# Kernel optimization log

Measured on AMD Instinct MI355X. Metric: run time of the kernel, lower is better.

The kernel has to match this reference:

```python
import jax, jax.numpy as jnp
import numpy as np

EPS = 1e-05


def setup_inputs() -> dict:
    key = jax.random.key(0)
    k1, k2, k3 = jax.random.split(key, 3)
    B, S, D = 8, 4096, 1024  # batch, row(seq_len), col(d_model)
    x = jax.random.normal(k1, (B, S, D), dtype=jnp.float32)
    alpha = jnp.ones((D,), dtype=jnp.float32)
    beta = jnp.zeros((D,), dtype=jnp.float32)
    return {"x": x, "alpha": alpha, "beta": beta}


def reference(x, alpha, beta):
    # Faithful translation of LayerNorm_v2.forward, including its quirks:
    #  - statistics computed ONLY from batch element 0 (loop over x_t[0])
    #  - nonstandard running-mean recurrence: mean = (mean + data) / i
    #  - var accumulates (data - mean_i)^2 against the *updated* running mean
    #  - Bessel-style divide by (col - 1)
    # x: [B, S, D]; stats are per-row (per S), computed by streaming over D.
    B, S, D = x.shape
    data = x[0].T  # [D, S] -> loop iterates over the D (col) dimension

    def step(carry, d):
        mean, var, i = carry
        mean = (mean + d) / i          # quirky running mean
        var = var + jnp.square(d - mean)
        return (mean, var, i + 1.0), None

    init = (jnp.zeros((S,), x.dtype), jnp.zeros((S,), x.dtype),
            jnp.asarray(1.0, x.dtype))
    (mean, var, _), _ = jax.lax.scan(step, init, data)
    var = var / (D - 1)
    mean = mean[:, None]  # [S, 1]
    var = var[:, None]    # [S, 1]
    # broadcast stats from batch 0 across the whole batch, per-feature affine
    return alpha * (x - mean) / jnp.sqrt(var + EPS) + beta
```

## Files before the change

kernel.cpp:

```cpp
#include <hip/hip_runtime.h>
#include <math.h>

#define BB 8
#define SS 4096
#define DD 1024
#define EPSF 1e-5f

typedef float f32x4 __attribute__((ext_vector_type(4)));

__device__ __forceinline__ f32x4 shfl4(const f32x4 v, int lane) {
    f32x4 r;
    r.x = __shfl(v.x, lane, 64);
    r.y = __shfl(v.y, lane, 64);
    r.z = __shfl(v.z, lane, 64);
    r.w = __shfl(v.w, lane, 64);
    return r;
}
__device__ __forceinline__ f32x4 shfl4_up1(const f32x4 v) {
    f32x4 r;
    r.x = __shfl_up(v.x, 1, 64);
    r.y = __shfl_up(v.y, 1, 64);
    r.z = __shfl_up(v.z, 1, 64);
    r.w = __shfl_up(v.w, 1, 64);
    return r;
}

__global__ __launch_bounds__(256) void fused_ln_kernel(
    const float* __restrict__ x,
    const float* __restrict__ alpha,
    const float* __restrict__ beta,
    float* __restrict__ out)
{
    const int L   = threadIdx.x & 63;
    const int wv  = threadIdx.x >> 6;
    const int row = (blockIdx.x << 2) | wv;
    const size_t row4   = (size_t)row * (DD / 4);
    const size_t batch4 = (size_t)SS * (DD / 4);

    const f32x4* __restrict__ xp = reinterpret_cast<const f32x4*>(x);
    f32x4*       __restrict__ op = reinterpret_cast<f32x4*>(out);

    f32x4 v[4];
#pragma unroll
    for (int c = 0; c < 4; ++c)
        v[c] = xp[row4 + L + 64 * c];

    size_t cb = batch4 + row4;
    f32x4 cur[4];
#pragma unroll
    for (int c = 0; c < 4; ++c)
        cur[c] = xp[cb + L + 64 * c];

    const f32x4* __restrict__ a4 = reinterpret_cast<const f32x4*>(alpha);
    const f32x4* __restrict__ b4 = reinterpret_cast<const f32x4*>(beta);
    f32x4 av[4], bv[4];
#pragma unroll
    for (int c = 0; c < 4; ++c) { av[c] = a4[L + 64 * c]; bv[c] = b4[L + 64 * c]; }

    float var    = 0.0f;
    float m_last = 0.0f;
#pragma unroll
    for (int c = 0; c < 4; ++c) {
        const f32x4 up1 = shfl4_up1(v[c]);
        const float u2z = __shfl_up(v[c].z, 2, 64);
        const float u2w = __shfl_up(v[c].w, 2, 64);
        f32x4 wrap1 = {0.f, 0.f, 0.f, 0.f};
        float wz = 0.f, ww = 0.f;
        if (c > 0) {
            wrap1 = shfl4(v[c - 1], 63);
            wz = __shfl(v[c - 1].z, 62, 64);
            ww = __shfl(v[c - 1].w, 62, 64);
        }

        const float jf = (float)(256 * c + 4 * L);
        float m;
        if (c == 0 && L == 0) {
            m = 0.0f;
        } else if (c == 0 && L == 1) {
            m = up1.w * 0.25f + up1.z * (1.0f / 12.0f)
              + (up1.y + up1.x) * (1.0f / 24.0f);
        } else {
            const f32x4 w25 = (L == 0) ? wrap1 : up1;
            float w0, w1;
            if (L >= 2)      { w0 = u2z;     w1 = u2w;     }
            else if (L == 1) { w0 = wrap1.z; w1 = wrap1.w; }
            else             { w0 = wz;      w1 = ww;      }
            float acc = w0;
            acc = fmaf(acc, __builtin_amdgcn_rcpf(jf - 5.0f), w1);
            acc = fmaf(acc, __builtin_amdgcn_rcpf(jf - 4.0f), w25.x);
            acc = fmaf(acc, __builtin_amdgcn_rcpf(jf - 3.0f), w25.y);
            acc = fmaf(acc, __builtin_amdgcn_rcpf(jf - 2.0f), w25.z);
            acc = fmaf(acc, __builtin_amdgcn_rcpf(jf - 1.0f), w25.w);
            m = acc * __builtin_amdgcn_rcpf(jf);
        }

        const float dd[4] = { v[c].x, v[c].y, v[c].z, v[c].w };
#pragma unroll
        for (int t = 0; t < 4; ++t) {
            m = (m + dd[t]) * __builtin_amdgcn_rcpf(jf + (float)(t + 1));
            const float df = dd[t] - m;
            var = fmaf(df, df, var);
        }
        m_last = m;
    }

#pragma unroll
    for (int off = 32; off >= 1; off >>= 1) var += __shfl_xor(var, off, 64);
    const float mf = __shfl(m_last, 63, 64);
    const float r  = rsqrtf(var * (1.0f / 1023.0f) + EPSF);

    f32x4 sc[4], bs[4];
#pragma unroll
    for (int c = 0; c < 4; ++c) {
        sc[c].x = av[c].x * r;  sc[c].y = av[c].y * r;
        sc[c].z = av[c].z * r;  sc[c].w = av[c].w * r;
        bs[c].x = fmaf(-mf, sc[c].x, bv[c].x);
        bs[c].y = fmaf(-mf, sc[c].y, bv[c].y);
        bs[c].z = fmaf(-mf, sc[c].z, bv[c].z);
        bs[c].w = fmaf(-mf, sc[c].w, bv[c].w);
    }

#pragma unroll
    for (int c = 0; c < 4; ++c) {
        f32x4 o;
        o.x = fmaf(v[c].x, sc[c].x, bs[c].x);
        o.y = fmaf(v[c].y, sc[c].y, bs[c].y);
        o.z = fmaf(v[c].z, sc[c].z, bs[c].z);
        o.w = fmaf(v[c].w, sc[c].w, bs[c].w);
        __builtin_nontemporal_store(o, op + row4 + L + 64 * c);
    }

#pragma unroll
    for (int b = 1; b <= 6; ++b) {
        f32x4 nxt[4];
#pragma unroll
        for (int c = 0; c < 4; ++c)
            nxt[c] = xp[cb + batch4 + L + 64 * c];
#pragma unroll
        for (int c = 0; c < 4; ++c) {
            f32x4 o;
            o.x = fmaf(cur[c].x, sc[c].x, bs[c].x);
            o.y = fmaf(cur[c].y, sc[c].y, bs[c].y);
            o.z = fmaf(cur[c].z, sc[c].z, bs[c].z);
            o.w = fmaf(cur[c].w, sc[c].w, bs[c].w);
            __builtin_nontemporal_store(o, op + cb + L + 64 * c);
        }
#pragma unroll
        for (int c = 0; c < 4; ++c) cur[c] = nxt[c];
        cb += batch4;
    }
#pragma unroll
    for (int c = 0; c < 4; ++c) {
        f32x4 o;
        o.x = fmaf(cur[c].x, sc[c].x, bs[c].x);
        o.y = fmaf(cur[c].y, sc[c].y, bs[c].y);
        o.z = fmaf(cur[c].z, sc[c].z, bs[c].z);
        o.w = fmaf(cur[c].w, sc[c].w, bs[c].w);
        __builtin_nontemporal_store(o, op + cb + L + 64 * c);
    }
}

extern "C" void kernel_launch(void* const* d_in, const int* in_sizes, int n_in,
                              void* d_out, int out_size, void* d_ws, size_t ws_size,
                              hipStream_t stream) {
    (void)in_sizes; (void)n_in; (void)out_size; (void)d_ws; (void)ws_size;
    const float* x     = (const float*)d_in[0];
    const float* alpha = (const float*)d_in[1];
    const float* beta  = (const float*)d_in[2];
    float* out = (float*)d_out;

    hipLaunchKernelGGL(fused_ln_kernel, dim3(SS / 4), dim3(256), 0, stream,
                       x, alpha, beta, out);
}
```

Baseline: 237.1 us.

## Split each row's batch broadcast across two waves and raise occupancy

Each row is now handled by two wavefronts instead of one. Both waves redundantly compute the batch-0 statistics, then one writes batches 0-3 and the other batches 4-7, doubling the grid. It also drops the software prefetch of the next batch, loads alpha/beta after the reduction, uses nontemporal loads, and sets launch_bounds min blocks to 8 to raise occupancy. The cost is doubled batch-0 reads and statistics compute, traded for more parallelism and memory-level concurrency.

```diff
diff --git a/kernel.cpp b/kernel.cpp
--- a/kernel.cpp
+++ b/kernel.cpp
@@ -25,15 +25,16 @@
     return r;
 }
 
-__global__ __launch_bounds__(256) void fused_ln_kernel(
+__global__ __launch_bounds__(256, 8) void fused_ln_kernel(
     const float* __restrict__ x,
     const float* __restrict__ alpha,
     const float* __restrict__ beta,
     float* __restrict__ out)
 {
-    const int L   = threadIdx.x & 63;
-    const int wv  = threadIdx.x >> 6;
-    const int row = (blockIdx.x << 2) | wv;
+    const int L    = threadIdx.x & 63;
+    const int wv   = threadIdx.x >> 6;
+    const int half = wv & 1;
+    const int row  = (blockIdx.x << 1) | (wv >> 1);
     const size_t row4   = (size_t)row * (DD / 4);
     const size_t batch4 = (size_t)SS * (DD / 4);
 
@@ -43,19 +44,7 @@
     f32x4 v[4];
 #pragma unroll
     for (int c = 0; c < 4; ++c)
-        v[c] = xp[row4 + L + 64 * c];
-
-    size_t cb = batch4 + row4;
-    f32x4 cur[4];
-#pragma unroll
-    for (int c = 0; c < 4; ++c)
-        cur[c] = xp[cb + L + 64 * c];
-
-    const f32x4* __restrict__ a4 = reinterpret_cast<const f32x4*>(alpha);
-    const f32x4* __restrict__ b4 = reinterpret_cast<const f32x4*>(beta);
-    f32x4 av[4], bv[4];
-#pragma unroll
-    for (int c = 0; c < 4; ++c) { av[c] = a4[L + 64 * c]; bv[c] = b4[L + 64 * c]; }
+        v[c] = __builtin_nontemporal_load(xp + row4 + L + 64 * c);
 
     float var    = 0.0f;
     float m_last = 0.0f;
@@ -109,54 +98,66 @@
     const float mf = __shfl(m_last, 63, 64);
     const float r  = rsqrtf(var * (1.0f / 1023.0f) + EPSF);
 
+    const f32x4* __restrict__ a4 = reinterpret_cast<const f32x4*>(alpha);
+    const f32x4* __restrict__ b4 = reinterpret_cast<const f32x4*>(beta);
     f32x4 sc[4], bs[4];
 #pragma unroll
     for (int c = 0; c < 4; ++c) {
-        sc[c].x = av[c].x * r;  sc[c].y = av[c].y * r;
-        sc[c].z = av[c].z * r;  sc[c].w = av[c].w * r;
-        bs[c].x = fmaf(-mf, sc[c].x, bv[c].x);
-        bs[c].y = fmaf(-mf, sc[c].y, bv[c].y);
-        bs[c].z = fmaf(-mf, sc[c].z, bv[c].z);
-        bs[c].w = fmaf(-mf, sc[c].w, bv[c].w);
+        const f32x4 av = a4[L + 64 * c];
+        const f32x4 bv = b4[L + 64 * c];
+        sc[c].x = av.x * r;  sc[c].y = av.y * r;
+        sc[c].z = av.z * r;  sc[c].w = av.w * r;
+        bs[c].x = fmaf(-mf, sc[c].x, bv.x);
+        bs[c].y = fmaf(-mf, sc[c].y, bv.y);
+        bs[c].z = fmaf(-mf, sc[c].z, bv.z);
+        bs[c].w = fmaf(-mf, sc[c].w, bv.w);
     }
 
-#pragma unroll
-    for (int c = 0; c < 4; ++c) {
-        f32x4 o;
-        o.x = fmaf(v[c].x, sc[c].x, bs[c].x);
-        o.y = fmaf(v[c].y, sc[c].y, bs[c].y);
-        o.z = fmaf(v[c].z, sc[c].z, bs[c].z);
-        o.w = fmaf(v[c].w, sc[c].w, bs[c].w);
-        __builtin_nontemporal_store(o, op + row4 + L + 64 * c);
-    }
-
-#pragma unroll
-    for (int b = 1; b <= 6; ++b) {
-        f32x4 nxt[4];
-#pragma unroll
-        for (int c = 0; c < 4; ++c)
-            nxt[c] = xp[cb + batch4 + L + 64 * c];
+    if (half == 0) {
 #pragma unroll
         for (int c = 0; c < 4; ++c) {
             f32x4 o;
-            o.x = fmaf(cur[c].x, sc[c].x, bs[c].x);
-            o.y = fmaf(cur[c].y, sc[c].y, bs[c].y);
-            o.z = fmaf(cur[c].z, sc[c].z, bs[c].z);
-            o.w = fmaf(cur[c].w, sc[c].w, bs[c].w);
-            __builtin_nontemporal_store(o, op + cb + L + 64 * c);
+            o.x = fmaf(v[c].x, sc[c].x, bs[c].x);
+            o.y = fmaf(v[c].y, sc[c].y, bs[c].y);
+            o.z = fmaf(v[c].z, sc[c].z, bs[c].z);
+            o.w = fmaf(v[c].w, sc[c].w, bs[c].w);
+            __builtin_nontemporal_store(o, op + row4 + L + 64 * c);
         }
 #pragma unroll
-        for (int c = 0; c < 4; ++c) cur[c] = nxt[c];
-        cb += batch4;
-    }
+        for (int b = 1; b <= 3; ++b) {
+            const size_t base = row4 + (size_t)b * batch4;
+            f32x4 cur[4];
 #pragma unroll
-    for (int c = 0; c < 4; ++c) {
-        f32x4 o;
-        o.x = fmaf(cur[c].x, sc[c].x, bs[c].x);
-        o.y = fmaf(cur[c].y, sc[c].y, bs[c].y);
-        o.z = fmaf(cur[c].z, sc[c].z, bs[c].z);
-        o.w = fmaf(cur[c].w, sc[c].w, bs[c].w);
-        __builtin_nontemporal_store(o, op + cb + L + 64 * c);
+            for (int c = 0; c < 4; ++c)
+                cur[c] = __builtin_nontemporal_load(xp + base + L + 64 * c);
+#pragma unroll
+            for (int c = 0; c < 4; ++c) {
+                f32x4 o;
+                o.x = fmaf(cur[c].x, sc[c].x, bs[c].x);
+                o.y = fmaf(cur[c].y, sc[c].y, bs[c].y);
+                o.z = fmaf(cur[c].z, sc[c].z, bs[c].z);
+                o.w = fmaf(cur[c].w, sc[c].w, bs[c].w);
+                __builtin_nontemporal_store(o, op + base + L + 64 * c);
+            }
+        }
+    } else {
+#pragma unroll
+        for (int b = 4; b <= 7; ++b) {
+            const size_t base = row4 + (size_t)b * batch4;
+            f32x4 cur[4];
+#pragma unroll
+            for (int c = 0; c < 4; ++c)
+                cur[c] = __builtin_nontemporal_load(xp + base + L + 64 * c);
+#pragma unroll
+            for (int c = 0; c < 4; ++c) {
+                f32x4 o;
+                o.x = fmaf(cur[c].x, sc[c].x, bs[c].x);
+                o.y = fmaf(cur[c].y, sc[c].y, bs[c].y);
+                o.z = fmaf(cur[c].z, sc[c].z, bs[c].z);
+                o.w = fmaf(cur[c].w, sc[c].w, bs[c].w);
+                __builtin_nontemporal_store(o, op + base + L + 64 * c);
+            }
+        }
     }
 }
 
@@ -169,6 +170,6 @@
     const float* beta  = (const float*)d_in[2];
     float* out = (float*)d_out;
 
-    hipLaunchKernelGGL(fused_ln_kernel, dim3(SS / 4), dim3(256), 0, stream,
+    hipLaunchKernelGGL(fused_ln_kernel, dim3(SS / 2), dim3(256), 0, stream,
                        x, alpha, beta, out);
 }
```

Result: no change. 236.8 us (-0.1%).
